# Optimization experiments

Hardware: AMD Instinct MI355X
Metric: run time of the kernel (lower is better)

The kernel has to match this reference:

```python
import jax, jax.numpy as jnp
import numpy as np

B, CIN, COUT, K, N = 4, 64, 64, 16, 32768


def setup_inputs() -> dict:
    key = jax.random.key(0)
    k1, k2, k3, k4, k5 = jax.random.split(key, 5)
    features = jax.random.normal(k1, (B, CIN, N), dtype=jnp.float32)
    neighborhood = jax.random.randint(k2, (B, K, N), 0, N, dtype=jnp.int32)
    positions = jax.random.normal(k3, (B, 3, N), dtype=jnp.float32)
    # kaiming-uniform-style init for params
    bt = float(np.sqrt(6.0 / (CIN * COUT)))
    weight_theta = jax.random.uniform(k4, (3, CIN, COUT), jnp.float32, -bt, bt)
    bb = float(np.sqrt(6.0 / CIN))
    weight_bias = jax.random.uniform(k5, (CIN, COUT), jnp.float32, -bb, bb)
    bias = jnp.zeros((COUT,), dtype=jnp.float32)
    return {"features": features, "weight_theta": weight_theta,
            "weight_bias": weight_bias, "bias": bias,
            "neighborhood": neighborhood, "positions": positions}


def reference(features, weight_theta, weight_bias, bias, neighborhood, positions):
    # features: [B, Cin, N]; neighborhood: [B, K, N]; positions: [B, 3, N]
    gather = jax.vmap(lambda f, nb: f[:, nb])  # [C, N], [K, N] -> [C, K, N]
    f_g = gather(features, neighborhood)           # [B, Cin, K, N]
    p_g = gather(positions, neighborhood)          # [B, 3, K, N]
    dp = p_g - positions[:, :, None, :]            # relative positions [B, 3, K, N]
    # position-dependent linear term: contract over neighbors first
    S = jnp.einsum('bckn,bdkn->bdcn', f_g, dp)     # [B, 3, Cin, N]
    fsum = f_g.sum(axis=2)                         # [B, Cin, N]
    out = (jnp.einsum('bdcn,dco->bon', S, weight_theta)
           + jnp.einsum('bcn,co->bon', fsum, weight_bias))  # [B, Cout, N]
    return out + bias[None, :, None]
```

## Files before the change

kernel.cpp:

```cpp
#include <hip/hip_runtime.h>
#include <hip/hip_bf16.h>

#define B_    4
#define CIN   64
#define COUT  64
#define KN    16
#define NPTS  32768
#define NPB   32

typedef __attribute__((ext_vector_type(8))) short short8;
typedef __attribute__((ext_vector_type(4))) float f32x4;
typedef __attribute__((ext_vector_type(4))) int   i32x4;

__global__ __launch_bounds__(256) void prep_all_kernel(
    const float* __restrict__ f,
    const float* __restrict__ pos,
    const float* __restrict__ wtheta,
    const float* __restrict__ wbias,
    __hip_bfloat16* __restrict__ ft,
    float4*         __restrict__ pt,
    __hip_bfloat16* __restrict__ Wt)
{
  __shared__ float tile[64][65];
  const int b    = blockIdx.y;
  const int n0   = blockIdx.x * 64;
  const int lane = threadIdx.x & 63;
  const int g    = threadIdx.x >> 6;
  const float* src = f + (size_t)b * CIN * NPTS + n0;
#pragma unroll
  for (int cc = 0; cc < 16; ++cc)
    tile[cc * 4 + g][lane] = src[(size_t)(cc * 4 + g) * NPTS + lane];
  __syncthreads();
  __hip_bfloat16* dst = ft + ((size_t)b * NPTS + n0) * CIN;
  const int nrow = threadIdx.x >> 5;
  const int c2   = (threadIdx.x & 31) * 2;
#pragma unroll
  for (int pass = 0; pass < 8; ++pass) {
    const int n = pass * 8 + nrow;
    __hip_bfloat162 v = __float22bfloat162_rn(
        make_float2(tile[c2][n], tile[c2 + 1][n]));
    *(__hip_bfloat162*)&dst[(size_t)n * CIN + c2] = v;
  }

  if (threadIdx.x < 64) {
    const int n = n0 + threadIdx.x;
    const float* ps = pos + (size_t)b * 3 * NPTS;
    float4 v;
    v.x = ps[n]; v.y = ps[NPTS + n]; v.z = ps[2 * NPTS + n]; v.w = 0.f;
    pt[(size_t)b * NPTS + n] = v;
  }

  if (b == 0 && blockIdx.x < 64) {
    const int t  = blockIdx.x * 256 + threadIdx.x;
    const int o  = t >> 8;
    const int cp = t & 255;
    const int c  = cp >> 2;
    const int d  = cp & 3;
    const float v = (d < 3) ? wtheta[((size_t)d * 64 + c) * 64 + o]
                            : wbias[(size_t)c * 64 + o];
    Wt[t] = __float2bfloat16(v);
  }
}

__global__ __launch_bounds__(256) void flex_fused_kernel(
    const __hip_bfloat16* __restrict__ ft,
    const float4* __restrict__ pt,
    const int*    __restrict__ nb,
    const __hip_bfloat16* __restrict__ Wt,
    const float*  __restrict__ bias,
    float*        __restrict__ out)
{
  __shared__ i32x4 recL[NPB * 17];
  __shared__ __hip_bfloat16 TL[NPB][272];

  const int t    = threadIdx.x;
  const int lane = t & 63;
  const int wv   = t >> 6;

  const int xcd = blockIdx.x & 7;
  const int b   = xcd >> 1;
  const int loc = (xcd & 1) * ((NPTS / NPB) >> 1) + (blockIdx.x >> 3);
  const int n0  = loc * NPB;

  const unsigned short* fpk = (const unsigned short*)ft + (size_t)b * NPTS * CIN;
  const float4* ptb = pt + (size_t)b * NPTS;
  const int*    nbb = nb + (size_t)b * KN * NPTS;

  {
    const int p  = t & 31;
    const int kk = t >> 5;
    const int n  = n0 + p;
    const float4 ctr = ptb[n];
#pragma unroll
    for (int kh = 0; kh < 2; ++kh) {
      const int k   = kk + kh * 8;
      const int idx = nbb[(size_t)k * NPTS + n];
      const float4 q = ptb[idx];
      i32x4 r;
      r.x = idx;
      r.y = __float_as_int(q.x - ctr.x);
      r.z = __float_as_int(q.y - ctr.y);
      r.w = __float_as_int(q.z - ctr.z);
      recL[p * 17 + k] = r;
    }
  }
  __syncthreads();

  {
    const unsigned* recD = (const unsigned*)recL;
    unsigned rv[8];
#pragma unroll
    for (int p = 0; p < 8; ++p)
      rv[p] = recD[(wv * 8 + p) * 68 + lane];

#pragma unroll
    for (int p = 0; p < 8; ++p) {
      float s0 = 0.f, s1 = 0.f, s2 = 0.f, fs = 0.f;
#pragma unroll
      for (int k = 0; k < KN; ++k) {
        const int   idx = __builtin_amdgcn_readlane(rv[p], 4 * k);
        const float dx  = __int_as_float(__builtin_amdgcn_readlane(rv[p], 4 * k + 1));
        const float dy  = __int_as_float(__builtin_amdgcn_readlane(rv[p], 4 * k + 2));
        const float dz  = __int_as_float(__builtin_amdgcn_readlane(rv[p], 4 * k + 3));
        const unsigned short u = fpk[(size_t)idx * CIN + lane];
        const float fv = __uint_as_float((unsigned)u << 16);
        fs += fv;
        s0 += fv * dx;
        s1 += fv * dy;
        s2 += fv * dz;
      }
      __hip_bfloat162 lo = __float22bfloat162_rn(make_float2(s0, s1));
      __hip_bfloat162 hi = __float22bfloat162_rn(make_float2(s2, fs));
      uint2 pk;
      pk.x = *(unsigned*)&lo;
      pk.y = *(unsigned*)&hi;
      *(uint2*)&TL[wv * 8 + p][lane * 4] = pk;
    }
  }
  __syncthreads();

  {
    const int col  = lane & 15;
    const int krow = lane >> 4;
    const unsigned short* wr =
        (const unsigned short*)Wt + (size_t)(wv * 16 + col) * 256 + krow * 8;
    short8 a[8];
#pragma unroll
    for (int kk = 0; kk < 8; ++kk) a[kk] = *(const short8*)(wr + kk * 32);

    f32x4 acc[2];
    acc[0] = (f32x4){0.f, 0.f, 0.f, 0.f};
    acc[1] = (f32x4){0.f, 0.f, 0.f, 0.f};
#pragma unroll
    for (int nt = 0; nt < 2; ++nt) {
      const unsigned short* tc =
          (const unsigned short*)&TL[nt * 16 + col][0] + krow * 8;
#pragma unroll
      for (int kk = 0; kk < 8; ++kk) {
        short8 bf = *(const short8*)(tc + kk * 32);
        acc[nt] = __builtin_amdgcn_mfma_f32_16x16x32_bf16(a[kk], bf, acc[nt], 0, 0, 0);
      }
    }

    const float4 bv = *(const float4*)(bias + wv * 16 + krow * 4);
    float* ob = out + ((size_t)b * COUT + wv * 16 + krow * 4) * NPTS + n0 + col;
#pragma unroll
    for (int r = 0; r < 4; ++r) {
      const float badd = (r == 0) ? bv.x : (r == 1) ? bv.y : (r == 2) ? bv.z : bv.w;
      float* orow = ob + (size_t)r * NPTS;
#pragma unroll
      for (int nt = 0; nt < 2; ++nt)
        __builtin_nontemporal_store(acc[nt][r] + badd, orow + nt * 16);
    }
  }
}

extern "C" void kernel_launch(void* const* d_in, const int* in_sizes, int n_in,
                              void* d_out, int out_size, void* d_ws, size_t ws_size,
                              hipStream_t stream) {
  const float* features = (const float*)d_in[0];
  const float* wtheta   = (const float*)d_in[1];
  const float* wbias    = (const float*)d_in[2];
  const float* bias     = (const float*)d_in[3];
  const int*   nb       = (const int*)  d_in[4];
  const float* pos      = (const float*)d_in[5];
  float* out = (float*)d_out;

  char* ws = (char*)d_ws;
  __hip_bfloat16* ft = (__hip_bfloat16*)ws;
  float4*         pt = (float4*)(ws + 16777216);
  __hip_bfloat16* Wt = (__hip_bfloat16*)(ws + 16777216 + 2097152);

  prep_all_kernel<<<dim3(NPTS / 64, B_), 256, 0, stream>>>(
      features, pos, wtheta, wbias, ft, pt, Wt);
  flex_fused_kernel<<<B_ * (NPTS / NPB), 256, 0, stream>>>(
      ft, pt, nb, Wt, bias, out);
}
```

Measured before the change: 147.3 us.

## Precompute packed fp16 neighbor records in prep and use fp16 dot2 accumulation

Moves the neighbor index gather and relative-position computation out of the main kernel into the prep kernel. There they are packed as 16-bit indices plus fp16 deltas into a 128-byte record per point. The main kernel reads these records directly instead of going through LDS and readlane, and accumulates with packed fp16 dot2 instructions. Features and weights switch from bf16 to fp16 so the MFMA uses the f16 variant. This cuts gather traffic and VALU work but narrows precision, and storing neighbor indices in 16 bits only works because N is 32768.

Measured after the change: 153.0 us. 3.8% more time.

```diff
diff --git a/kernel.cpp b/kernel.cpp
--- a/kernel.cpp
+++ b/kernel.cpp
@@ -1,5 +1,4 @@
 #include <hip/hip_runtime.h>
-#include <hip/hip_bf16.h>
 
 #define B_    4
 #define CIN   64
@@ -8,46 +7,86 @@
 #define NPTS  32768
 #define NPB   32
 
-typedef __attribute__((ext_vector_type(8))) short short8;
-typedef __attribute__((ext_vector_type(4))) float f32x4;
-typedef __attribute__((ext_vector_type(4))) int   i32x4;
+typedef __fp16 f16;
+typedef __attribute__((ext_vector_type(8))) __fp16 half8;
+typedef __attribute__((ext_vector_type(2))) __fp16 half2v;
+typedef __attribute__((ext_vector_type(4))) float  f32x4;
+
+static __device__ __forceinline__ half2v uint_as_h2(unsigned u) {
+  union { unsigned u; half2v h; } c; c.u = u; return c.h;
+}
+static __device__ __forceinline__ unsigned h2_as_uint(half2v h) {
+  union { unsigned u; half2v h; } c; c.h = h; return c.u;
+}
+
+static __device__ __forceinline__ float dot2_acc(half2v a, half2v b, float acc) {
+#if __has_builtin(__builtin_amdgcn_fdot2)
+  return __builtin_amdgcn_fdot2(a, b, acc, false);
+#else
+  return acc + (float)a.x * (float)b.x + (float)a.y * (float)b.y;
+#endif
+}
 
 __global__ __launch_bounds__(256) void prep_all_kernel(
     const float* __restrict__ f,
     const float* __restrict__ pos,
+    const int*   __restrict__ nb,
     const float* __restrict__ wtheta,
     const float* __restrict__ wbias,
-    __hip_bfloat16* __restrict__ ft,
-    float4*         __restrict__ pt,
-    __hip_bfloat16* __restrict__ Wt)
+    f16*         __restrict__ ft,
+    unsigned*    __restrict__ recG,
+    f16*         __restrict__ Wt)
 {
-  __shared__ float tile[64][65];
+  __shared__ union {
+    float    tile[64][65];
+    unsigned recs[64][33];
+  } sm;
+
   const int b    = blockIdx.y;
   const int n0   = blockIdx.x * 64;
   const int lane = threadIdx.x & 63;
   const int g    = threadIdx.x >> 6;
+
   const float* src = f + (size_t)b * CIN * NPTS + n0;
 #pragma unroll
   for (int cc = 0; cc < 16; ++cc)
-    tile[cc * 4 + g][lane] = src[(size_t)(cc * 4 + g) * NPTS + lane];
-  __syncthreads();
-  __hip_bfloat16* dst = ft + ((size_t)b * NPTS + n0) * CIN;
+    sm.tile[cc * 4 + g][lane] = src[(size_t)(cc * 4 + g) * NPTS + lane];
+  __syncthreads();
+  f16* dst = ft + ((size_t)b * NPTS + n0) * CIN;
   const int nrow = threadIdx.x >> 5;
   const int c2   = (threadIdx.x & 31) * 2;
 #pragma unroll
   for (int pass = 0; pass < 8; ++pass) {
     const int n = pass * 8 + nrow;
-    __hip_bfloat162 v = __float22bfloat162_rn(
-        make_float2(tile[c2][n], tile[c2 + 1][n]));
-    *(__hip_bfloat162*)&dst[(size_t)n * CIN + c2] = v;
-  }
-
-  if (threadIdx.x < 64) {
-    const int n = n0 + threadIdx.x;
-    const float* ps = pos + (size_t)b * 3 * NPTS;
-    float4 v;
-    v.x = ps[n]; v.y = ps[NPTS + n]; v.z = ps[2 * NPTS + n]; v.w = 0.f;
-    pt[(size_t)b * NPTS + n] = v;
+    half2v v = __builtin_amdgcn_cvt_pkrtz(sm.tile[c2][n], sm.tile[c2 + 1][n]);
+    *(half2v*)&dst[(size_t)n * CIN + c2] = v;
+  }
+  __syncthreads();
+
+  {
+    const int p  = threadIdx.x & 63;
+    const int kh = threadIdx.x >> 6;
+    const int n  = n0 + p;
+    const float* pb = pos + (size_t)b * 3 * NPTS;
+    const float cx = pb[n], cy = pb[NPTS + n], cz = pb[2 * NPTS + n];
+    const int* nbb = nb + (size_t)b * KN * NPTS + n;
+    int idx[4]; float dx[4], dy[4], dz[4];
+#pragma unroll
+    for (int j = 0; j < 4; ++j) {
+      const int k = kh * 4 + j;
+      idx[j] = nbb[(size_t)k * NPTS];
+      dx[j] = pb[idx[j]] - cx;
+      dy[j] = pb[NPTS + idx[j]] - cy;
+      dz[j] = pb[2 * NPTS + idx[j]] - cz;
+    }
+#pragma unroll
+    for (int jj = 0; jj < 2; ++jj) {
+      const int dw = kh * 2 + jj;
+      sm.recs[p][dw] = (unsigned)idx[2 * jj] | ((unsigned)idx[2 * jj + 1] << 16);
+      sm.recs[p][8  + dw] = h2_as_uint(__builtin_amdgcn_cvt_pkrtz(dx[2 * jj], dx[2 * jj + 1]));
+      sm.recs[p][16 + dw] = h2_as_uint(__builtin_amdgcn_cvt_pkrtz(dy[2 * jj], dy[2 * jj + 1]));
+      sm.recs[p][24 + dw] = h2_as_uint(__builtin_amdgcn_cvt_pkrtz(dz[2 * jj], dz[2 * jj + 1]));
+    }
   }
 
   if (b == 0 && blockIdx.x < 64) {
@@ -58,107 +97,88 @@
     const int d  = cp & 3;
     const float v = (d < 3) ? wtheta[((size_t)d * 64 + c) * 64 + o]
                             : wbias[(size_t)c * 64 + o];
-    Wt[t] = __float2bfloat16(v);
+    Wt[t] = (f16)v;
+  }
+  __syncthreads();
+
+  {
+    const int p = threadIdx.x >> 2;
+    const int q = threadIdx.x & 3;
+    unsigned* gdst = recG + ((size_t)b * NPTS + n0) * 32 + (size_t)threadIdx.x * 8;
+#pragma unroll
+    for (int j = 0; j < 8; ++j) gdst[j] = sm.recs[p][q * 8 + j];
   }
 }
 
 __global__ __launch_bounds__(256) void flex_fused_kernel(
-    const __hip_bfloat16* __restrict__ ft,
-    const float4* __restrict__ pt,
-    const int*    __restrict__ nb,
-    const __hip_bfloat16* __restrict__ Wt,
-    const float*  __restrict__ bias,
-    float*        __restrict__ out)
+    const unsigned short* __restrict__ ftu,
+    const unsigned* __restrict__ recG,
+    const f16*      __restrict__ Wt,
+    const float*    __restrict__ bias,
+    float*          __restrict__ out)
 {
-  __shared__ i32x4 recL[NPB * 17];
-  __shared__ __hip_bfloat16 TL[NPB][272];
+  __shared__ f16 TL[NPB][272];
 
   const int t    = threadIdx.x;
   const int lane = t & 63;
-  const int wv   = t >> 6;
+  const int wv   = __builtin_amdgcn_readfirstlane(t >> 6);
 
   const int xcd = blockIdx.x & 7;
   const int b   = xcd >> 1;
   const int loc = (xcd & 1) * ((NPTS / NPB) >> 1) + (blockIdx.x >> 3);
   const int n0  = loc * NPB;
 
-  const unsigned short* fpk = (const unsigned short*)ft + (size_t)b * NPTS * CIN;
-  const float4* ptb = pt + (size_t)b * NPTS;
-  const int*    nbb = nb + (size_t)b * KN * NPTS;
-
-  {
-    const int p  = t & 31;
-    const int kk = t >> 5;
-    const int n  = n0 + p;
-    const float4 ctr = ptb[n];
-#pragma unroll
-    for (int kh = 0; kh < 2; ++kh) {
-      const int k   = kk + kh * 8;
-      const int idx = nbb[(size_t)k * NPTS + n];
-      const float4 q = ptb[idx];
-      i32x4 r;
-      r.x = idx;
-      r.y = __float_as_int(q.x - ctr.x);
-      r.z = __float_as_int(q.y - ctr.y);
-      r.w = __float_as_int(q.z - ctr.z);
-      recL[p * 17 + k] = r;
-    }
-  }
-  __syncthreads();
-
-  {
-    const unsigned* recD = (const unsigned*)recL;
-    unsigned rv[8];
-#pragma unroll
-    for (int p = 0; p < 8; ++p)
-      rv[p] = recD[(wv * 8 + p) * 68 + lane];
-
-#pragma unroll
-    for (int p = 0; p < 8; ++p) {
-      float s0 = 0.f, s1 = 0.f, s2 = 0.f, fs = 0.f;
-#pragma unroll
-      for (int k = 0; k < KN; ++k) {
-        const int   idx = __builtin_amdgcn_readlane(rv[p], 4 * k);
-        const float dx  = __int_as_float(__builtin_amdgcn_readlane(rv[p], 4 * k + 1));
-        const float dy  = __int_as_float(__builtin_amdgcn_readlane(rv[p], 4 * k + 2));
-        const float dz  = __int_as_float(__builtin_amdgcn_readlane(rv[p], 4 * k + 3));
-        const unsigned short u = fpk[(size_t)idx * CIN + lane];
-        const float fv = __uint_as_float((unsigned)u << 16);
-        fs += fv;
-        s0 += fv * dx;
-        s1 += fv * dy;
-        s2 += fv * dz;
-      }
-      __hip_bfloat162 lo = __float22bfloat162_rn(make_float2(s0, s1));
-      __hip_bfloat162 hi = __float22bfloat162_rn(make_float2(s2, fs));
-      uint2 pk;
-      pk.x = *(unsigned*)&lo;
-      pk.y = *(unsigned*)&hi;
-      *(uint2*)&TL[wv * 8 + p][lane * 4] = pk;
-    }
+  const char* fpk = (const char*)(ftu + (size_t)b * NPTS * CIN);
+  const unsigned* recp = recG + ((size_t)b * NPTS + n0 + wv * 8) * 32;
+  const half2v one2 = {(__fp16)1.0f, (__fp16)1.0f};
+
+#pragma unroll
+  for (int p = 0; p < 8; ++p) {
+    const unsigned* rp = recp + p * 32;
+    unsigned iw[8];
+#pragma unroll
+    for (int j = 0; j < 8; ++j) iw[j] = rp[j];
+    unsigned fvv[16];
+#pragma unroll
+    for (int k = 0; k < 16; ++k) {
+      const unsigned off =
+          (((k & 1) ? (iw[k >> 1] >> 16) : (iw[k >> 1] & 0xffffu)) << 7);
+      fvv[k] = *(const unsigned short*)(fpk + off + lane * 2);
+    }
+    float s0 = 0.f, s1 = 0.f, s2 = 0.f, fs = 0.f;
+#pragma unroll
+    for (int kk = 0; kk < 8; ++kk) {
+      const half2v fp = uint_as_h2(fvv[2 * kk] | (fvv[2 * kk + 1] << 16));
+      s0 = dot2_acc(uint_as_h2(rp[8  + kk]), fp, s0);
+      s1 = dot2_acc(uint_as_h2(rp[16 + kk]), fp, s1);
+      s2 = dot2_acc(uint_as_h2(rp[24 + kk]), fp, s2);
+      fs = dot2_acc(one2, fp, fs);
+    }
+    uint2 pk;
+    pk.x = h2_as_uint(__builtin_amdgcn_cvt_pkrtz(s0, s1));
+    pk.y = h2_as_uint(__builtin_amdgcn_cvt_pkrtz(s2, fs));
+    *(uint2*)&TL[wv * 8 + p][lane * 4] = pk;
   }
   __syncthreads();
 
   {
     const int col  = lane & 15;
     const int krow = lane >> 4;
-    const unsigned short* wr =
-        (const unsigned short*)Wt + (size_t)(wv * 16 + col) * 256 + krow * 8;
-    short8 a[8];
-#pragma unroll
-    for (int kk = 0; kk < 8; ++kk) a[kk] = *(const short8*)(wr + kk * 32);
+    const f16* wr = Wt + (size_t)(wv * 16 + col) * 256 + krow * 8;
+    half8 a[8];
+#pragma unroll
+    for (int kk = 0; kk < 8; ++kk) a[kk] = *(const half8*)(wr + kk * 32);
 
     f32x4 acc[2];
     acc[0] = (f32x4){0.f, 0.f, 0.f, 0.f};
     acc[1] = (f32x4){0.f, 0.f, 0.f, 0.f};
 #pragma unroll
     for (int nt = 0; nt < 2; ++nt) {
-      const unsigned short* tc =
-          (const unsigned short*)&TL[nt * 16 + col][0] + krow * 8;
+      const f16* tc = &TL[nt * 16 + col][0] + krow * 8;
 #pragma unroll
       for (int kk = 0; kk < 8; ++kk) {
-        short8 bf = *(const short8*)(tc + kk * 32);
-        acc[nt] = __builtin_amdgcn_mfma_f32_16x16x32_bf16(a[kk], bf, acc[nt], 0, 0, 0);
+        half8 bf = *(const half8*)(tc + kk * 32);
+        acc[nt] = __builtin_amdgcn_mfma_f32_16x16x32_f16(a[kk], bf, acc[nt], 0, 0, 0);
       }
     }
 
@@ -187,12 +207,12 @@
   float* out = (float*)d_out;
 
   char* ws = (char*)d_ws;
-  __hip_bfloat16* ft = (__hip_bfloat16*)ws;
-  float4*         pt = (float4*)(ws + 16777216);
-  __hip_bfloat16* Wt = (__hip_bfloat16*)(ws + 16777216 + 2097152);
+  f16*      ft  = (f16*)ws;
+  f16*      Wt  = (f16*)(ws + 16777216);
+  unsigned* rec = (unsigned*)(ws + 16777216 + 32768);
 
   prep_all_kernel<<<dim3(NPTS / 64, B_), 256, 0, stream>>>(
-      features, pos, wtheta, wbias, ft, pt, Wt);
+      features, pos, nb, wtheta, wbias, ft, rec, Wt);
   flex_fused_kernel<<<B_ * (NPTS / NPB), 256, 0, stream>>>(
-      ft, pt, nb, Wt, bias, out);
-}
+      (const unsigned short*)ft, rec, Wt, bias, out);
+}
```
